# Performance work log

Hardware: AMD Instinct MI355X
Metric: run time of the kernel (lower is better)

The kernel has to match this reference:

```python
import jax, jax.numpy as jnp
import numpy as np

N = 100000   # nodes
E = 1600000  # edges
D = 128      # input_dim == hidden_dim
G = 64       # graphs in batch
EPS = 1e-5


def setup_inputs() -> dict:
    key = jax.random.key(0)
    ks = jax.random.split(key, 16)
    s = 1.0 / np.sqrt(D)
    inp = {
        "x": jax.random.normal(ks[0], (N, D), jnp.float32),
        "edge_index": jax.random.randint(ks[1], (2, E), 0, N, jnp.int64),
        "batch": jnp.sort(jax.random.randint(ks[2], (N,), 0, G, jnp.int64)),
        # 4 blocks x 2 SAGEConv layers = 8 convs, all DxD
        "Wl": jax.random.normal(ks[3], (8, D, D), jnp.float32) * s,
        "bl": jnp.zeros((8, D), jnp.float32),
        "Wr": jax.random.normal(ks[4], (8, D, D), jnp.float32) * s,
        "gamma": jnp.ones((4, D), jnp.float32),
        "beta": jnp.zeros((4, D), jnp.float32),
        # classifier: 2D -> D -> D//2 -> 1
        "W1": jax.random.normal(ks[5], (2 * D, D), jnp.float32) / np.sqrt(2 * D),
        "b1": jnp.zeros((D,), jnp.float32),
        "W2": jax.random.normal(ks[6], (D, D // 2), jnp.float32) * s,
        "b2": jnp.zeros((D // 2,), jnp.float32),
        "W3": jax.random.normal(ks[7], (D // 2, 1), jnp.float32) / np.sqrt(D // 2),
        "b3": jnp.zeros((1,), jnp.float32),
    }
    return inp


def _sage_conv(h, src, dst, inv_deg, W_l, b_l, W_r):
    # mean-aggregate neighbor features (messages flow src -> dst)
    agg = jax.ops.segment_sum(h[src], dst, num_segments=N) * inv_deg
    return agg @ W_l + b_l + h @ W_r


def _forward(x, edge_index, batch, Wl, bl, Wr, gamma, beta, W1, b1, W2, b2, W3, b3):
    src, dst = edge_index[0], edge_index[1]
    deg = jax.ops.segment_sum(jnp.ones((E,), x.dtype), dst, num_segments=N)
    inv_deg = (1.0 / jnp.maximum(deg, 1.0))[:, None]  # [N,1]

    h = x
    for blk in range(4):
        # GraphSAGE(in, hid, num_layers=2): conv -> relu -> conv
        h = _sage_conv(h, src, dst, inv_deg, Wl[2 * blk], bl[2 * blk], Wr[2 * blk])
        h = jax.nn.relu(h)
        h = _sage_conv(h, src, dst, inv_deg, Wl[2 * blk + 1], bl[2 * blk + 1], Wr[2 * blk + 1])
        # BatchNorm1d over nodes (training-mode batch statistics, biased var)
        mu = jnp.mean(h, axis=0)
        var = jnp.var(h, axis=0)
        h = (h - mu) * jax.lax.rsqrt(var + EPS) * gamma[blk] + beta[blk]
        h = jax.nn.relu(h)  # dropout is identity in eval mode

    # global mean / max pool over graph ids
    cnt = jax.ops.segment_sum(jnp.ones((N,), h.dtype), batch, num_segments=G)
    x_mean = jax.ops.segment_sum(h, batch, num_segments=G) / jnp.maximum(cnt, 1.0)[:, None]
    x_max = jax.ops.segment_max(h, batch, num_segments=G)
    g = jnp.concatenate([x_mean, x_max], axis=1)  # [G, 2D]

    g = jax.nn.relu(g @ W1 + b1)
    g = jax.nn.relu(g @ W2 + b2)
    return g @ W3 + b3  # [G, 1]


def reference(x, edge_index, batch, Wl, bl, Wr, gamma, beta, W1, b1, W2, b2, W3, b3):
    return _forward(x, edge_index, batch, Wl, bl, Wr, gamma, beta, W1, b1, W2, b2, W3, b3)
```

## Files before the change

### kernel.cpp

```cpp
#include <hip/hip_runtime.h>
#include <hip/hip_bf16.h>
#include <math.h>

#define NN 100000
#define NE 1600000
#define DIM 128
#define NG 64
#define EPSBN 1e-5f
#define NBLK 782
#define SORT_WIN 12500

typedef unsigned int u32;
typedef unsigned short u16;
typedef __attribute__((ext_vector_type(8))) short bf8_t;
typedef __attribute__((ext_vector_type(4))) float f4_t;
typedef __attribute__((ext_vector_type(4))) unsigned short u16x4;
#define MFMA(a, b, c) __builtin_amdgcn_mfma_f32_16x16x32_bf16((a), (b), (c), 0, 0, 0)

__device__ __forceinline__ u16 f2bf(float f) {
    u32 u = __float_as_uint(f);
    u32 r = u + 0x7FFFu + ((u >> 16) & 1u);
    return (u16)(r >> 16);
}
__device__ __forceinline__ float bf2f(u16 h) { return __uint_as_float(((u32)h) << 16); }

__global__ void k_deg_hist(const int* __restrict__ ei, int* __restrict__ deg) {
    int e = blockIdx.x * blockDim.x + threadIdx.x;
    if (e < NE) atomicAdd(&deg[ei[NE + e]], 1);
}

#define SCAN_B 256
__global__ void k_scan1(const int* __restrict__ deg, int* __restrict__ row_start,
                        int* __restrict__ bsum, float* __restrict__ inv_deg) {
    __shared__ int s[SCAN_B];
    int t = threadIdx.x;
    int i = blockIdx.x * SCAN_B + t;
    int v = (i < NN) ? deg[i] : 0;
    if (i < NN) inv_deg[i] = 1.0f / (float)(v > 1 ? v : 1);
    s[t] = v;
    for (int off = 1; off < SCAN_B; off <<= 1) {
        __syncthreads();
        int x = (t >= off) ? s[t - off] : 0;
        __syncthreads();
        s[t] += x;
    }
    if (i < NN) row_start[i + 1] = s[t];
    if (t == SCAN_B - 1) bsum[blockIdx.x] = s[t];
}

__global__ void k_scan2(int* __restrict__ bsum, int nb) {
    __shared__ int s[512];
    int t = threadIdx.x;
    int v = (t < nb) ? bsum[t] : 0;
    s[t] = v;
    for (int off = 1; off < 512; off <<= 1) {
        __syncthreads();
        int x = (t >= off) ? s[t - off] : 0;
        __syncthreads();
        s[t] += x;
    }
    if (t < nb) bsum[t] = s[t] - v;
}

__global__ void k_scan3(int* __restrict__ row_start, const int* __restrict__ bsum,
                        int* __restrict__ cursor) {
    int i = blockIdx.x * blockDim.x + threadIdx.x;
    if (i < NN) {
        int v = row_start[i + 1] + bsum[i / SCAN_B];
        row_start[i + 1] = v;
        if (i + 1 < NN) cursor[i + 1] = v;
    }
    if (i == 0) { row_start[0] = 0; cursor[0] = 0; }
}

__global__ void k_sort(const int* __restrict__ ei, int* __restrict__ cursor,
                       int* __restrict__ sorted_src) {
    int e = blockIdx.x * 256 + threadIdx.x;
    int s = ei[e];
    int d = ei[NE + e];
    int w = d / SORT_WIN;
#pragma unroll
    for (int p = 0; p < 8; ++p) {
        if (w == p) {
            int pos = atomicAdd(&cursor[d], 1);
            sorted_src[pos] = s;
        }
        __syncthreads();
    }
}

__global__ void k_bounds(const int* __restrict__ batch, int* __restrict__ gs) {
    int g = threadIdx.x;
    if (g > NG) return;
    int lo = 0, hi = NN;
    while (lo < hi) {
        int mid = (lo + hi) >> 1;
        if (batch[mid] < g) lo = mid + 1; else hi = mid;
    }
    gs[g] = lo;
}

__global__ void k_split_x(const float* __restrict__ x, u16* __restrict__ Xh,
                          u16* __restrict__ Xl) {
    int idx = blockIdx.x * 256 + threadIdx.x;
    int base = idx * 4;
    float4 v = *reinterpret_cast<const float4*>(&x[base]);
    u16x4 hi, lo;
    float vv[4] = {v.x, v.y, v.z, v.w};
#pragma unroll
    for (int j = 0; j < 4; j++) {
        u16 h = f2bf(vv[j]);
        hi[j] = h;
        lo[j] = f2bf(vv[j] - bf2f(h));
    }
    *reinterpret_cast<u16x4*>(&Xh[base]) = hi;
    *reinterpret_cast<u16x4*>(&Xl[base]) = lo;
}

__global__ void k_prep_w(const float* __restrict__ Wl, const float* __restrict__ Wr,
                         u16* __restrict__ Wth, u16* __restrict__ Wtl) {
    int idx = blockIdx.x * 256 + threadIdx.x;
    int k = idx & 255;
    int col = (idx >> 8) & 127;
    int c = idx >> 15;
    float v = (k < 128) ? Wl[(c * 128 + k) * 128 + col] : Wr[(c * 128 + (k - 128)) * 128 + col];
    u16 h = f2bf(v);
    Wth[idx] = h;
    Wtl[idx] = f2bf(v - bf2f(h));
}

__global__ void k_aggregate(const u16* __restrict__ Hh,
                            const int* __restrict__ row_start, const int* __restrict__ ssrc,
                            const float* __restrict__ inv_deg,
                            u16* __restrict__ Ah, u16* __restrict__ Al) {
    int wid = blockIdx.x * 4 + (threadIdx.x >> 6);
    int lane = threadIdx.x & 63;
    int half = lane >> 5;
    int cl = lane & 31;
    if (wid >= NN) return;
    int beg = row_start[wid], end = row_start[wid + 1];
    int n = end - beg;
    float a0 = 0.f, a1 = 0.f, a2 = 0.f, a3 = 0.f;
    for (int base = 0; base < n; base += 64) {
        int rem = n - base;
        int idx = beg + base + (lane < rem ? lane : 0);
        int sv = ssrc[idx];
        int m = rem < 64 ? rem : 64;
        int j = 0;
        for (; j + 4 <= m; j += 4) {
            int sA = __shfl(sv, j + half);
            int sB = __shfl(sv, j + 2 + half);
            uint2 vA = *reinterpret_cast<const uint2*>(
                reinterpret_cast<const u32*>(Hh + (size_t)sA * DIM) + cl * 2);
            uint2 vB = *reinterpret_cast<const uint2*>(
                reinterpret_cast<const u32*>(Hh + (size_t)sB * DIM) + cl * 2);
            a0 += __uint_as_float(vA.x << 16) + __uint_as_float(vB.x << 16);
            a1 += __uint_as_float(vA.x & 0xFFFF0000u) + __uint_as_float(vB.x & 0xFFFF0000u);
            a2 += __uint_as_float(vA.y << 16) + __uint_as_float(vB.y << 16);
            a3 += __uint_as_float(vA.y & 0xFFFF0000u) + __uint_as_float(vB.y & 0xFFFF0000u);
        }
        for (; j < m; j += 2) {
            if (j + half < m) {
                int s0 = __shfl(sv, j + half);
                uint2 v = *reinterpret_cast<const uint2*>(
                    reinterpret_cast<const u32*>(Hh + (size_t)s0 * DIM) + cl * 2);
                a0 += __uint_as_float(v.x << 16);
                a1 += __uint_as_float(v.x & 0xFFFF0000u);
                a2 += __uint_as_float(v.y << 16);
                a3 += __uint_as_float(v.y & 0xFFFF0000u);
            }
        }
    }
    a0 += __shfl_down(a0, 32);
    a1 += __shfl_down(a1, 32);
    a2 += __shfl_down(a2, 32);
    a3 += __shfl_down(a3, 32);
    if (half == 0) {
        float sc = inv_deg[wid];
        a0 *= sc; a1 *= sc; a2 *= sc; a3 *= sc;
        u16 h0 = f2bf(a0), h1 = f2bf(a1), h2 = f2bf(a2), h3 = f2bf(a3);
        u16 l0 = f2bf(a0 - bf2f(h0)), l1 = f2bf(a1 - bf2f(h1));
        u16 l2 = f2bf(a2 - bf2f(h2)), l3 = f2bf(a3 - bf2f(h3));
        uint2 hv = make_uint2((u32)h0 | ((u32)h1 << 16), (u32)h2 | ((u32)h3 << 16));
        uint2 lv = make_uint2((u32)l0 | ((u32)l1 << 16), (u32)l2 | ((u32)l3 << 16));
        *reinterpret_cast<uint2*>(Ah + (size_t)wid * DIM + cl * 4) = hv;
        *reinterpret_cast<uint2*>(Al + (size_t)wid * DIM + cl * 4) = lv;
    }
}

template <bool RELU, bool STATS>
__global__ __launch_bounds__(256) void k_gemm(
    const u16* __restrict__ A1h, const u16* __restrict__ A1l,
    const u16* __restrict__ A2h, const u16* __restrict__ A2l,
    const u16* __restrict__ Wth, const u16* __restrict__ Wtl,
    const float* __restrict__ bias,
    u16* __restrict__ Oh, u16* __restrict__ Ol,
    float* __restrict__ partials) {
    __shared__ float cs[128], cq[128];
    int t = threadIdx.x;
    if (STATS) {
        if (t < 128) { cs[t] = 0.f; cq[t] = 0.f; }
        __syncthreads();
    }
    int w = t >> 6, l = t & 63;
    int rl = l & 15, kg = l >> 4;
    int rbase = blockIdx.x * 128 + w * 32;
    int row0 = rbase + rl, row1 = rbase + 16 + rl;
    int row0c = min(row0, NN - 1), row1c = min(row1, NN - 1);

    f4_t acc[2][8];
#pragma unroll
    for (int i = 0; i < 2; i++)
#pragma unroll
        for (int j = 0; j < 8; j++) acc[i][j] = (f4_t){0.f, 0.f, 0.f, 0.f};

#pragma unroll
    for (int ks = 0; ks < 4; ++ks) {
        int k0 = ks * 32 + kg * 8;
        bf8_t a0h = *reinterpret_cast<const bf8_t*>(A1h + row0c * DIM + k0);
        bf8_t a0l = *reinterpret_cast<const bf8_t*>(A1l + row0c * DIM + k0);
        bf8_t a1h = *reinterpret_cast<const bf8_t*>(A1h + row1c * DIM + k0);
        bf8_t a1l = *reinterpret_cast<const bf8_t*>(A1l + row1c * DIM + k0);
#pragma unroll
        for (int cf = 0; cf < 8; ++cf) {
            int wo = (cf * 16 + rl) * 256 + k0;
            bf8_t bh = *reinterpret_cast<const bf8_t*>(Wth + wo);
            bf8_t bl_ = *reinterpret_cast<const bf8_t*>(Wtl + wo);
            acc[0][cf] = MFMA(a0h, bh, acc[0][cf]);
            acc[0][cf] = MFMA(a0h, bl_, acc[0][cf]);
            acc[0][cf] = MFMA(a0l, bh, acc[0][cf]);
            acc[1][cf] = MFMA(a1h, bh, acc[1][cf]);
            acc[1][cf] = MFMA(a1h, bl_, acc[1][cf]);
            acc[1][cf] = MFMA(a1l, bh, acc[1][cf]);
        }
    }
#pragma unroll
    for (int ks = 0; ks < 4; ++ks) {
        int k0 = ks * 32 + kg * 8;
        bf8_t a0h = *reinterpret_cast<const bf8_t*>(A2h + row0c * DIM + k0);
        bf8_t a0l = *reinterpret_cast<const bf8_t*>(A2l + row0c * DIM + k0);
        bf8_t a1h = *reinterpret_cast<const bf8_t*>(A2h + row1c * DIM + k0);
        bf8_t a1l = *reinterpret_cast<const bf8_t*>(A2l + row1c * DIM + k0);
#pragma unroll
        for (int cf = 0; cf < 8; ++cf) {
            int wo = (cf * 16 + rl) * 256 + 128 + k0;
            bf8_t bh = *reinterpret_cast<const bf8_t*>(Wth + wo);
            bf8_t bl_ = *reinterpret_cast<const bf8_t*>(Wtl + wo);
            acc[0][cf] = MFMA(a0h, bh, acc[0][cf]);
            acc[0][cf] = MFMA(a0h, bl_, acc[0][cf]);
            acc[0][cf] = MFMA(a0l, bh, acc[0][cf]);
            acc[1][cf] = MFMA(a1h, bh, acc[1][cf]);
            acc[1][cf] = MFMA(a1h, bl_, acc[1][cf]);
            acc[1][cf] = MFMA(a1l, bh, acc[1][cf]);
        }
    }

#pragma unroll
    for (int rf = 0; rf < 2; ++rf) {
        int rb = rbase + rf * 16 + kg * 4;
#pragma unroll
        for (int cf = 0; cf < 8; ++cf) {
            int col = cf * 16 + rl;
            float bv = bias[col];
            float s = 0.f, q = 0.f;
#pragma unroll
            for (int i = 0; i < 4; ++i) {
                int row = rb + i;
                float v = acc[rf][cf][i] + bv;
                if (RELU) v = fmaxf(v, 0.f);
                if (row < NN) {
                    u16 hi = f2bf(v);
                    Oh[row * DIM + col] = hi;
                    Ol[row * DIM + col] = f2bf(v - bf2f(hi));
                    if (STATS) { s += v; q += v * v; }
                }
            }
            if (STATS) {
                s += __shfl_xor(s, 16); s += __shfl_xor(s, 32);
                q += __shfl_xor(q, 16); q += __shfl_xor(q, 32);
                if (l < 16) {
                    atomicAdd(&cs[col], s);
                    atomicAdd(&cq[col], q);
                }
            }
        }
    }
    if (STATS) {
        __syncthreads();
        partials[blockIdx.x * 256 + t] = (t < 128) ? cs[t] : cq[t - 128];
    }
}

__global__ void k_bn_r1(const float* __restrict__ partials, float* __restrict__ colpart) {
    int t = threadIdx.x;
    int b = blockIdx.x;
    int b0 = b * 25, b1 = min(b0 + 25, NBLK);
    float s = 0.f;
    for (int i = b0; i < b1; ++i) s += partials[i * 256 + t];
    colpart[b * 256 + t] = s;
}

__global__ void k_bn_r2(const float* __restrict__ colpart, const float* __restrict__ gamma,
                        const float* __restrict__ beta, float* __restrict__ scaleshift) {
    __shared__ float sm[256];
    int t = threadIdx.x;
    float s = 0.f;
#pragma unroll
    for (int b = 0; b < 32; ++b) s += colpart[b * 256 + t];
    sm[t] = s;
    __syncthreads();
    if (t < 128) {
        float mu = sm[t] * (1.0f / NN);
        float var = sm[t + 128] * (1.0f / NN) - mu * mu;
        float sc = rsqrtf(var + EPSBN) * gamma[t];
        scaleshift[t] = sc;
        scaleshift[t + 128] = beta[t] - mu * sc;
    }
}

__global__ void k_bn_apply(u16* __restrict__ Hh, u16* __restrict__ Hl,
                           const float* __restrict__ scaleshift) {
    int idx = blockIdx.x * 256 + threadIdx.x;
    int base = idx * 4;
    int col = base & 127;
    u16x4 hi = *reinterpret_cast<const u16x4*>(Hh + base);
    u16x4 lo = *reinterpret_cast<const u16x4*>(Hl + base);
#pragma unroll
    for (int j = 0; j < 4; j++) {
        float v = bf2f(hi[j]) + bf2f(lo[j]);
        v = fmaxf(v * scaleshift[col + j] + scaleshift[128 + col + j], 0.f);
        u16 h = f2bf(v);
        hi[j] = h;
        lo[j] = f2bf(v - bf2f(h));
    }
    *reinterpret_cast<u16x4*>(Hh + base) = hi;
    *reinterpret_cast<u16x4*>(Hl + base) = lo;
}

__global__ void k_pool(const u16* __restrict__ Hh, const u16* __restrict__ Hl,
                       const int* __restrict__ gs, float* __restrict__ pSum,
                       float* __restrict__ pMax) {
    int g = blockIdx.x >> 3, slice = blockIdx.x & 7;
    int s0 = gs[g], s1 = gs[g + 1];
    int len = s1 - s0;
    int chunk = (len + 7) >> 3;
    int r0 = s0 + slice * chunk;
    int r1 = min(r0 + chunk, s1);
    int t = threadIdx.x;
    int c2 = (t & 63) * 2, half = t >> 6;
    float sa = 0.f, sb = 0.f, ma = 0.f, mb = 0.f;
    for (int r = r0 + half; r < r1; r += 4) {
        u32 h2 = *reinterpret_cast<const u32*>(Hh + r * DIM + c2);
        u32 l2 = *reinterpret_cast<const u32*>(Hl + r * DIM + c2);
        float v0 = __uint_as_float(h2 << 16) + __uint_as_float(l2 << 16);
        float v1 = __uint_as_float(h2 & 0xFFFF0000u) + __uint_as_float(l2 & 0xFFFF0000u);
        sa += v0; sb += v1;
        ma = fmaxf(ma, v0); mb = fmaxf(mb, v1);
    }
    __shared__ float ls[4][128], lm[4][128];
    ls[half][c2] = sa; ls[half][c2 + 1] = sb;
    lm[half][c2] = ma; lm[half][c2 + 1] = mb;
    __syncthreads();
    if (t < 128) {
        float s = ls[0][t] + ls[1][t] + ls[2][t] + ls[3][t];
        float m = fmaxf(fmaxf(lm[0][t], lm[1][t]), fmaxf(lm[2][t], lm[3][t]));
        atomicAdd(&pSum[g * DIM + t], s);
        atomicMax((int*)&pMax[g * DIM + t], __float_as_int(m));
    }
}

__global__ void k_mlp(const float* __restrict__ pSum, const float* __restrict__ pMax,
                      const int* __restrict__ gs,
                      const float* __restrict__ W1, const float* __restrict__ b1,
                      const float* __restrict__ W2, const float* __restrict__ b2,
                      const float* __restrict__ W3, const float* __restrict__ b3,
                      float* __restrict__ out) {
    __shared__ float g[256], y1[128], y2[64];
    int gi = blockIdx.x;
    int t = threadIdx.x;
    int cnt = gs[gi + 1] - gs[gi];
    float inv = 1.0f / fmaxf((float)cnt, 1.0f);
    g[t] = pSum[gi * DIM + t] * inv;
    g[128 + t] = pMax[gi * DIM + t];
    __syncthreads();
    float a = b1[t];
    for (int k = 0; k < 256; k++) a += g[k] * W1[k * 128 + t];
    y1[t] = fmaxf(a, 0.f);
    __syncthreads();
    if (t < 64) {
        float a2 = b2[t];
        for (int k = 0; k < 128; k++) a2 += y1[k] * W2[k * 64 + t];
        y2[t] = fmaxf(a2, 0.f);
    }
    __syncthreads();
    if (t < 64) {
        float p = y2[t] * W3[t];
#pragma unroll
        for (int off = 32; off; off >>= 1) p += __shfl_down(p, off);
        if (t == 0) out[gi] = p + b3[0];
    }
}

extern "C" void kernel_launch(void* const* d_in, const int* in_sizes, int n_in,
                              void* d_out, int out_size, void* d_ws, size_t ws_size,
                              hipStream_t stream) {
    const float* x     = (const float*)d_in[0];
    const int*   ei    = (const int*)d_in[1];
    const int*   batch = (const int*)d_in[2];
    const float* Wl    = (const float*)d_in[3];
    const float* bl    = (const float*)d_in[4];
    const float* Wr    = (const float*)d_in[5];
    const float* gamma = (const float*)d_in[6];
    const float* beta  = (const float*)d_in[7];
    const float* W1    = (const float*)d_in[8];
    const float* b1    = (const float*)d_in[9];
    const float* W2    = (const float*)d_in[10];
    const float* b2    = (const float*)d_in[11];
    const float* W3    = (const float*)d_in[12];
    const float* b3    = (const float*)d_in[13];
    float* out = (float*)d_out;

    char* p = (char*)d_ws;
    size_t off = 0;
    auto alloc = [&](size_t bytes) -> void* {
        void* r = p + off;
        off += (bytes + 255) & ~(size_t)255;
        return r;
    };
    const size_t HB = (size_t)NN * DIM * 2;
    u16* Xh   = (u16*)alloc(HB);
    u16* Xl   = (u16*)alloc(HB);
    u16* hAh  = (u16*)alloc(HB);
    u16* hAl  = (u16*)alloc(HB);
    u16* aggh = (u16*)alloc(HB);
    u16* aggl = (u16*)alloc(HB);
    int*   ssrc      = (int*)alloc((size_t)NE * 4);
    u16*   Wth       = (u16*)alloc((size_t)8 * 128 * 256 * 2);
    u16*   Wtl       = (u16*)alloc((size_t)8 * 128 * 256 * 2);
    float* partials  = (float*)alloc((size_t)NBLK * 256 * 4);
    float* colpart   = (float*)alloc(32 * 256 * 4);
    int*   deg       = (int*)alloc(NN * 4);
    float* inv_deg   = (float*)alloc(NN * 4);
    int*   row_start = (int*)alloc((NN + 1) * 4);
    int*   cursor    = (int*)alloc(NN * 4);
    int*   bsum      = (int*)alloc(512 * 4);
    int*   gs        = (int*)alloc((NG + 1) * 4);
    float* scaleshift= (float*)alloc(256 * 4);
    float* pSum      = (float*)alloc(NG * DIM * 4);
    float* pMax      = (float*)alloc(NG * DIM * 4);

    const int nbN = (NN + 255) / 256;
    const int nbE = (NE + 255) / 256;
    const int nbQ = NN * DIM / 4 / 256;
    const int aggGrid = (NN + 3) / 4;

    hipMemsetAsync(deg, 0, NN * 4, stream);
    k_deg_hist<<<nbE, 256, 0, stream>>>(ei, deg);
    k_scan1<<<nbN, 256, 0, stream>>>(deg, row_start, bsum, inv_deg);
    k_scan2<<<1, 512, 0, stream>>>(bsum, nbN);
    k_scan3<<<nbN, 256, 0, stream>>>(row_start, bsum, cursor);
    k_sort<<<nbE, 256, 0, stream>>>(ei, cursor, ssrc);
    k_bounds<<<1, 128, 0, stream>>>(batch, gs);

    k_split_x<<<nbQ, 256, 0, stream>>>(x, Xh, Xl);
    k_prep_w<<<8 * 128 * 256 / 256, 256, 0, stream>>>(Wl, Wr, Wth, Wtl);

    for (int b = 0; b < 4; b++) {
        int c0 = 2 * b, c1 = 2 * b + 1;
        const u16* W0h = Wth + (size_t)c0 * 128 * 256;
        const u16* W0l = Wtl + (size_t)c0 * 128 * 256;
        const u16* W1h = Wth + (size_t)c1 * 128 * 256;
        const u16* W1l = Wtl + (size_t)c1 * 128 * 256;
        k_aggregate<<<aggGrid, 256, 0, stream>>>(Xh, row_start, ssrc, inv_deg, aggh, aggl);
        k_gemm<true, false><<<NBLK, 256, 0, stream>>>(aggh, aggl, Xh, Xl, W0h, W0l,
                                                      bl + c0 * DIM, hAh, hAl, partials);
        k_aggregate<<<aggGrid, 256, 0, stream>>>(hAh, row_start, ssrc, inv_deg, aggh, aggl);
        k_gemm<false, true><<<NBLK, 256, 0, stream>>>(aggh, aggl, hAh, hAl, W1h, W1l,
                                                      bl + c1 * DIM, Xh, Xl, partials);
        k_bn_r1<<<32, 256, 0, stream>>>(partials, colpart);
        k_bn_r2<<<1, 256, 0, stream>>>(colpart, gamma + b * DIM, beta + b * DIM, scaleshift);
        k_bn_apply<<<nbQ, 256, 0, stream>>>(Xh, Xl, scaleshift);
    }

    hipMemsetAsync(pSum, 0, NG * DIM * 4, stream);
    hipMemsetAsync(pMax, 0, NG * DIM * 4, stream);
    k_pool<<<NG * 8, 256, 0, stream>>>(Xh, Xl, gs, pSum, pMax);
    k_mlp<<<NG, 128, 0, stream>>>(pSum, pMax, gs, W1, b1, W2, b2, W3, b3, out);
}
```

Before: 1.702 ms.

## Fuse BatchNorm apply into consumers and replace edge sort with binned counting sort

Removes the standalone BN-apply pass. The scale/shift plus ReLU is now applied lazily inside the next block's aggregate gather, the first GEMM's self-feature load and the pooling kernel, which saves a full read-write pass over the hidden state per block. The edge CSR build is also restructured into a block-level counting sort that bins edges by destination window, then runs degree counting and scatter per bin. This replaces the old global atomic histogram and the barrier-serialized sort kernel. The costs are extra FLOPs in every gather (the affine is recomputed per edge), more small launches, and pooling that reads only the high bf16 half, which lowers precision slightly.

```diff
diff --git a/kernel.cpp b/kernel.cpp
--- a/kernel.cpp
+++ b/kernel.cpp
@@ -9,6 +9,8 @@
 #define EPSBN 1e-5f
 #define NBLK 782
 #define SORT_WIN 12500
+#define NBINBLK 6250
+#define DSL 64
 
 typedef unsigned int u32;
 typedef unsigned short u16;
@@ -24,9 +26,85 @@
 }
 __device__ __forceinline__ float bf2f(u16 h) { return __uint_as_float(((u32)h) << 16); }
 
-__global__ void k_deg_hist(const int* __restrict__ ei, int* __restrict__ deg) {
-    int e = blockIdx.x * blockDim.x + threadIdx.x;
-    if (e < NE) atomicAdd(&deg[ei[NE + e]], 1);
+__global__ void k_bin_cnt(const int* __restrict__ ei, int* __restrict__ blkcnt) {
+    __shared__ int c[8];
+    int t = threadIdx.x;
+    if (t < 8) c[t] = 0;
+    __syncthreads();
+    int e = blockIdx.x * 256 + t;
+    int d = ei[NE + e];
+    atomicAdd(&c[d / SORT_WIN], 1);
+    __syncthreads();
+    if (t < 8) blkcnt[blockIdx.x * 8 + t] = c[t];
+}
+
+__global__ void k_bin_scan(const int* __restrict__ blkcnt, int* __restrict__ blkoff,
+                           int* __restrict__ wtotal) {
+    __shared__ int ps[256];
+    int w = blockIdx.x, t = threadIdx.x;
+    const int PER = (NBINBLK + 255) / 256;
+    int s = 0;
+    for (int i = 0; i < PER; ++i) {
+        int b = t * PER + i;
+        if (b < NBINBLK) s += blkcnt[b * 8 + w];
+    }
+    ps[t] = s;
+    for (int off = 1; off < 256; off <<= 1) {
+        __syncthreads();
+        int x = (t >= off) ? ps[t - off] : 0;
+        __syncthreads();
+        ps[t] += x;
+    }
+    __syncthreads();
+    int run = (t ? ps[t - 1] : 0);
+    for (int i = 0; i < PER; ++i) {
+        int b = t * PER + i;
+        if (b < NBINBLK) { blkoff[b * 8 + w] = run; run += blkcnt[b * 8 + w]; }
+    }
+    if (t == 255) wtotal[w] = ps[255];
+}
+
+__global__ void k_bin_start(const int* __restrict__ wtotal, int* __restrict__ binStart) {
+    if (threadIdx.x == 0) {
+        int a = 0;
+        for (int w = 0; w < 8; ++w) { binStart[w] = a; a += wtotal[w]; }
+        binStart[8] = a;
+    }
+}
+
+__global__ void k_bin_place(const int* __restrict__ ei, const int* __restrict__ blkoff,
+                            const int* __restrict__ binStart, int2* __restrict__ binned) {
+    __shared__ int base[8];
+    int t = threadIdx.x;
+    if (t < 8) base[t] = binStart[t] + blkoff[blockIdx.x * 8 + t];
+    __syncthreads();
+    int e = blockIdx.x * 256 + t;
+    int s = ei[e], d = ei[NE + e];
+    int pos = atomicAdd(&base[d / SORT_WIN], 1);
+    binned[pos] = make_int2(s, d);
+}
+
+__global__ void k_deg2(const int2* __restrict__ binned, const int* __restrict__ binStart,
+                       int* __restrict__ deg) {
+    int w = blockIdx.x & 7, sl = blockIdx.x >> 3;
+    int b0 = binStart[w], b1 = binStart[w + 1];
+    int chunk = (b1 - b0 + DSL - 1) / DSL;
+    int r0 = b0 + sl * chunk, r1 = min(r0 + chunk, b1);
+    for (int i = r0 + threadIdx.x; i < r1; i += 256)
+        atomicAdd(&deg[binned[i].y], 1);
+}
+
+__global__ void k_scatter(const int2* __restrict__ binned, const int* __restrict__ binStart,
+                          int* __restrict__ cursor, int* __restrict__ sorted_src) {
+    int w = blockIdx.x & 7, sl = blockIdx.x >> 3;
+    int b0 = binStart[w], b1 = binStart[w + 1];
+    int chunk = (b1 - b0 + DSL - 1) / DSL;
+    int r0 = b0 + sl * chunk, r1 = min(r0 + chunk, b1);
+    for (int i = r0 + threadIdx.x; i < r1; i += 256) {
+        int2 e = binned[i];
+        int pos = atomicAdd(&cursor[e.y], 1);
+        sorted_src[pos] = e.x;
+    }
 }
 
 #define SCAN_B 256
@@ -71,22 +149,6 @@
         if (i + 1 < NN) cursor[i + 1] = v;
     }
     if (i == 0) { row_start[0] = 0; cursor[0] = 0; }
-}
-
-__global__ void k_sort(const int* __restrict__ ei, int* __restrict__ cursor,
-                       int* __restrict__ sorted_src) {
-    int e = blockIdx.x * 256 + threadIdx.x;
-    int s = ei[e];
-    int d = ei[NE + e];
-    int w = d / SORT_WIN;
-#pragma unroll
-    for (int p = 0; p < 8; ++p) {
-        if (w == p) {
-            int pos = atomicAdd(&cursor[d], 1);
-            sorted_src[pos] = s;
-        }
-        __syncthreads();
-    }
 }
 
 __global__ void k_bounds(const int* __restrict__ batch, int* __restrict__ gs) {
@@ -129,18 +191,39 @@
     Wtl[idx] = f2bf(v - bf2f(h));
 }
 
+template <int AFF>
 __global__ void k_aggregate(const u16* __restrict__ Hh,
                             const int* __restrict__ row_start, const int* __restrict__ ssrc,
-                            const float* __restrict__ inv_deg,
+                            const float* __restrict__ inv_deg, const float* __restrict__ ss,
                             u16* __restrict__ Ah, u16* __restrict__ Al) {
     int wid = blockIdx.x * 4 + (threadIdx.x >> 6);
     int lane = threadIdx.x & 63;
     int half = lane >> 5;
     int cl = lane & 31;
     if (wid >= NN) return;
+    float sc0 = 0.f, sc1 = 0.f, sc2 = 0.f, sc3 = 0.f;
+    float sh0 = 0.f, sh1 = 0.f, sh2 = 0.f, sh3 = 0.f;
+    if (AFF) {
+        float4 s4 = *reinterpret_cast<const float4*>(ss + cl * 4);
+        float4 h4 = *reinterpret_cast<const float4*>(ss + 128 + cl * 4);
+        sc0 = s4.x; sc1 = s4.y; sc2 = s4.z; sc3 = s4.w;
+        sh0 = h4.x; sh1 = h4.y; sh2 = h4.z; sh3 = h4.w;
+    }
     int beg = row_start[wid], end = row_start[wid + 1];
     int n = end - beg;
     float a0 = 0.f, a1 = 0.f, a2 = 0.f, a3 = 0.f;
+#define ACCUM(vv)                                                                   \
+    {                                                                               \
+        float t0 = __uint_as_float((vv).x << 16);                                   \
+        float t1 = __uint_as_float((vv).x & 0xFFFF0000u);                           \
+        float t2 = __uint_as_float((vv).y << 16);                                   \
+        float t3 = __uint_as_float((vv).y & 0xFFFF0000u);                           \
+        if (AFF) {                                                                  \
+            t0 = fmaxf(t0 * sc0 + sh0, 0.f); t1 = fmaxf(t1 * sc1 + sh1, 0.f);       \
+            t2 = fmaxf(t2 * sc2 + sh2, 0.f); t3 = fmaxf(t3 * sc3 + sh3, 0.f);       \
+        }                                                                           \
+        a0 += t0; a1 += t1; a2 += t2; a3 += t3;                                     \
+    }
     for (int base = 0; base < n; base += 64) {
         int rem = n - base;
         int idx = beg + base + (lane < rem ? lane : 0);
@@ -154,23 +237,18 @@
                 reinterpret_cast<const u32*>(Hh + (size_t)sA * DIM) + cl * 2);
             uint2 vB = *reinterpret_cast<const uint2*>(
                 reinterpret_cast<const u32*>(Hh + (size_t)sB * DIM) + cl * 2);
-            a0 += __uint_as_float(vA.x << 16) + __uint_as_float(vB.x << 16);
-            a1 += __uint_as_float(vA.x & 0xFFFF0000u) + __uint_as_float(vB.x & 0xFFFF0000u);
-            a2 += __uint_as_float(vA.y << 16) + __uint_as_float(vB.y << 16);
-            a3 += __uint_as_float(vA.y & 0xFFFF0000u) + __uint_as_float(vB.y & 0xFFFF0000u);
+            ACCUM(vA); ACCUM(vB);
         }
         for (; j < m; j += 2) {
             if (j + half < m) {
                 int s0 = __shfl(sv, j + half);
                 uint2 v = *reinterpret_cast<const uint2*>(
                     reinterpret_cast<const u32*>(Hh + (size_t)s0 * DIM) + cl * 2);
-                a0 += __uint_as_float(v.x << 16);
-                a1 += __uint_as_float(v.x & 0xFFFF0000u);
-                a2 += __uint_as_float(v.y << 16);
-                a3 += __uint_as_float(v.y & 0xFFFF0000u);
+                ACCUM(v);
             }
         }
     }
+#undef ACCUM
     a0 += __shfl_down(a0, 32);
     a1 += __shfl_down(a1, 32);
     a2 += __shfl_down(a2, 32);
@@ -188,12 +266,24 @@
     }
 }
 
-template <bool RELU, bool STATS>
+__device__ __forceinline__ void affine_split(bf8_t& h, bf8_t& l,
+                                             const float* __restrict__ ss, int k0) {
+#pragma unroll
+    for (int j = 0; j < 8; ++j) {
+        float v = bf2f((u16)h[j]) + bf2f((u16)l[j]);
+        v = fmaxf(v * ss[k0 + j] + ss[128 + k0 + j], 0.f);
+        u16 hh = f2bf(v);
+        h[j] = (short)hh;
+        l[j] = (short)f2bf(v - bf2f(hh));
+    }
+}
+
+template <bool RELU, bool STATS, bool AFF2>
 __global__ __launch_bounds__(256) void k_gemm(
     const u16* __restrict__ A1h, const u16* __restrict__ A1l,
     const u16* __restrict__ A2h, const u16* __restrict__ A2l,
     const u16* __restrict__ Wth, const u16* __restrict__ Wtl,
-    const float* __restrict__ bias,
+    const float* __restrict__ bias, const float* __restrict__ ss,
     u16* __restrict__ Oh, u16* __restrict__ Ol,
     float* __restrict__ partials) {
     __shared__ float cs[128], cq[128];
@@ -241,6 +331,10 @@
         bf8_t a0l = *reinterpret_cast<const bf8_t*>(A2l + row0c * DIM + k0);
         bf8_t a1h = *reinterpret_cast<const bf8_t*>(A2h + row1c * DIM + k0);
         bf8_t a1l = *reinterpret_cast<const bf8_t*>(A2l + row1c * DIM + k0);
+        if (AFF2) {
+            affine_split(a0h, a0l, ss, k0);
+            affine_split(a1h, a1l, ss, k0);
+        }
 #pragma unroll
         for (int cf = 0; cf < 8; ++cf) {
             int wo = (cf * 16 + rl) * 256 + 128 + k0;
@@ -318,28 +412,9 @@
     }
 }
 
-__global__ void k_bn_apply(u16* __restrict__ Hh, u16* __restrict__ Hl,
-                           const float* __restrict__ scaleshift) {
-    int idx = blockIdx.x * 256 + threadIdx.x;
-    int base = idx * 4;
-    int col = base & 127;
-    u16x4 hi = *reinterpret_cast<const u16x4*>(Hh + base);
-    u16x4 lo = *reinterpret_cast<const u16x4*>(Hl + base);
-#pragma unroll
-    for (int j = 0; j < 4; j++) {
-        float v = bf2f(hi[j]) + bf2f(lo[j]);
-        v = fmaxf(v * scaleshift[col + j] + scaleshift[128 + col + j], 0.f);
-        u16 h = f2bf(v);
-        hi[j] = h;
-        lo[j] = f2bf(v - bf2f(h));
-    }
-    *reinterpret_cast<u16x4*>(Hh + base) = hi;
-    *reinterpret_cast<u16x4*>(Hl + base) = lo;
-}
-
-__global__ void k_pool(const u16* __restrict__ Hh, const u16* __restrict__ Hl,
-                       const int* __restrict__ gs, float* __restrict__ pSum,
-                       float* __restrict__ pMax) {
+__global__ void k_pool(const u16* __restrict__ Hh, const int* __restrict__ gs,
+                       const float* __restrict__ ss,
+                       float* __restrict__ pSum, float* __restrict__ pMax) {
     int g = blockIdx.x >> 3, slice = blockIdx.x & 7;
     int s0 = gs[g], s1 = gs[g + 1];
     int len = s1 - s0;
@@ -348,12 +423,13 @@
     int r1 = min(r0 + chunk, s1);
     int t = threadIdx.x;
     int c2 = (t & 63) * 2, half = t >> 6;
+    float sc0 = ss[c2], sc1 = ss[c2 + 1];
+    float sh0 = ss[128 + c2], sh1 = ss[128 + c2 + 1];
     float sa = 0.f, sb = 0.f, ma = 0.f, mb = 0.f;
     for (int r = r0 + half; r < r1; r += 4) {
         u32 h2 = *reinterpret_cast<const u32*>(Hh + r * DIM + c2);
-        u32 l2 = *reinterpret_cast<const u32*>(Hl + r * DIM + c2);
-        float v0 = __uint_as_float(h2 << 16) + __uint_as_float(l2 << 16);
-        float v1 = __uint_as_float(h2 & 0xFFFF0000u) + __uint_as_float(l2 & 0xFFFF0000u);
+        float v0 = fmaxf(__uint_as_float(h2 << 16) * sc0 + sh0, 0.f);
+        float v1 = fmaxf(__uint_as_float(h2 & 0xFFFF0000u) * sc1 + sh1, 0.f);
         sa += v0; sb += v1;
         ma = fmaxf(ma, v0); mb = fmaxf(mb, v1);
     }
@@ -445,21 +521,29 @@
     int*   cursor    = (int*)alloc(NN * 4);
     int*   bsum      = (int*)alloc(512 * 4);
     int*   gs        = (int*)alloc((NG + 1) * 4);
-    float* scaleshift= (float*)alloc(256 * 4);
+    int*   blkcnt    = (int*)alloc((size_t)NBINBLK * 8 * 4);
+    int*   blkoff    = (int*)alloc((size_t)NBINBLK * 8 * 4);
+    int*   wtotal    = (int*)alloc(8 * 4);
+    int*   binStart  = (int*)alloc(9 * 4);
+    float* ssb       = (float*)alloc(4 * 256 * 4);
     float* pSum      = (float*)alloc(NG * DIM * 4);
     float* pMax      = (float*)alloc(NG * DIM * 4);
+    int2*  binned    = (int2*)aggh;
 
     const int nbN = (NN + 255) / 256;
-    const int nbE = (NE + 255) / 256;
     const int nbQ = NN * DIM / 4 / 256;
     const int aggGrid = (NN + 3) / 4;
 
     hipMemsetAsync(deg, 0, NN * 4, stream);
-    k_deg_hist<<<nbE, 256, 0, stream>>>(ei, deg);
+    k_bin_cnt<<<NBINBLK, 256, 0, stream>>>(ei, blkcnt);
+    k_bin_scan<<<8, 256, 0, stream>>>(blkcnt, blkoff, wtotal);
+    k_bin_start<<<1, 64, 0, stream>>>(wtotal, binStart);
+    k_bin_place<<<NBINBLK, 256, 0, stream>>>(ei, blkoff, binStart, binned);
+    k_deg2<<<8 * DSL, 256, 0, stream>>>(binned, binStart, deg);
     k_scan1<<<nbN, 256, 0, stream>>>(deg, row_start, bsum, inv_deg);
     k_scan2<<<1, 512, 0, stream>>>(bsum, nbN);
     k_scan3<<<nbN, 256, 0, stream>>>(row_start, bsum, cursor);
-    k_sort<<<nbE, 256, 0, stream>>>(ei, cursor, ssrc);
+    k_scatter<<<8 * DSL, 256, 0, stream>>>(binned, binStart, cursor, ssrc);
     k_bounds<<<1, 128, 0, stream>>>(batch, gs);
 
     k_split_x<<<nbQ, 256, 0, stream>>>(x, Xh, Xl);
@@ -471,19 +555,29 @@
         const u16* W0l = Wtl + (size_t)c0 * 128 * 256;
         const u16* W1h = Wth + (size_t)c1 * 128 * 256;
         const u16* W1l = Wtl + (size_t)c1 * 128 * 256;
-        k_aggregate<<<aggGrid, 256, 0, stream>>>(Xh, row_start, ssrc, inv_deg, aggh, aggl);
-        k_gemm<true, false><<<NBLK, 256, 0, stream>>>(aggh, aggl, Xh, Xl, W0h, W0l,
-                                                      bl + c0 * DIM, hAh, hAl, partials);
-        k_aggregate<<<aggGrid, 256, 0, stream>>>(hAh, row_start, ssrc, inv_deg, aggh, aggl);
-        k_gemm<false, true><<<NBLK, 256, 0, stream>>>(aggh, aggl, hAh, hAl, W1h, W1l,
-                                                      bl + c1 * DIM, Xh, Xl, partials);
+        const float* ssPrev = ssb + (size_t)(b > 0 ? b - 1 : 0) * 256;
+        if (b == 0) {
+            k_aggregate<0><<<aggGrid, 256, 0, stream>>>(Xh, row_start, ssrc, inv_deg,
+                                                        ssPrev, aggh, aggl);
+            k_gemm<true, false, false><<<NBLK, 256, 0, stream>>>(
+                aggh, aggl, Xh, Xl, W0h, W0l, bl + c0 * DIM, ssPrev, hAh, hAl, partials);
+        } else {
+            k_aggregate<1><<<aggGrid, 256, 0, stream>>>(Xh, row_start, ssrc, inv_deg,
+                                                        ssPrev, aggh, aggl);
+            k_gemm<true, false, true><<<NBLK, 256, 0, stream>>>(
+                aggh, aggl, Xh, Xl, W0h, W0l, bl + c0 * DIM, ssPrev, hAh, hAl, partials);
+        }
+        k_aggregate<0><<<aggGrid, 256, 0, stream>>>(hAh, row_start, ssrc, inv_deg,
+                                                    ssPrev, aggh, aggl);
+        k_gemm<false, true, false><<<NBLK, 256, 0, stream>>>(
+            aggh, aggl, hAh, hAl, W1h, W1l, bl + c1 * DIM, ssPrev, Xh, Xl, partials);
         k_bn_r1<<<32, 256, 0, stream>>>(partials, colpart);
-        k_bn_r2<<<1, 256, 0, stream>>>(colpart, gamma + b * DIM, beta + b * DIM, scaleshift);
-        k_bn_apply<<<nbQ, 256, 0, stream>>>(Xh, Xl, scaleshift);
+        k_bn_r2<<<1, 256, 0, stream>>>(colpart, gamma + b * DIM, beta + b * DIM,
+                                       ssb + (size_t)b * 256);
     }
 
     hipMemsetAsync(pSum, 0, NG * DIM * 4, stream);
     hipMemsetAsync(pMax, 0, NG * DIM * 4, stream);
-    k_pool<<<NG * 8, 256, 0, stream>>>(Xh, Xl, gs, pSum, pMax);
+    k_pool<<<NG * 8, 256, 0, stream>>>(Xh, gs, ssb + 3 * 256, pSum, pMax);
     k_mlp<<<NG, 128, 0, stream>>>(pSum, pMax, gs, W1, b1, W2, b2, W3, b3, out);
 }
```

Measured after the change: 1.662 ms. -2.4%, faster.
